# Optimization experiments

Hardware: AMD Instinct MI355X
Metric: run time of the kernel (lower is better)

## Reference

```python
import jax, jax.numpy as jnp
import numpy as np

EPS_NORM = 1e-12  # torch F.normalize eps


def _resize_bilinear_ac(x, H, W):
    # Bilinear resize with align_corners=True on NCHW tensor x.
    h, w = x.shape[-2], x.shape[-1]
    ys = jnp.linspace(0.0, h - 1.0, H)
    xs = jnp.linspace(0.0, w - 1.0, W)
    y0 = jnp.floor(ys).astype(jnp.int32); y1 = jnp.minimum(y0 + 1, h - 1)
    x0 = jnp.floor(xs).astype(jnp.int32); x1 = jnp.minimum(x0 + 1, w - 1)
    wy = (ys - y0).astype(x.dtype)[None, None, :, None]
    wx = (xs - x0).astype(x.dtype)
    rows = x[:, :, y0, :] * (1 - wy) + x[:, :, y1, :] * wy  # (B,C,H,w)
    return rows[:, :, :, x0] * (1 - wx) + rows[:, :, :, x1] * wx  # (B,C,H,W)


def _icc(p, b):
    # p: (b, 19, hw) row-stochastic over hw.
    # M[i, j] = KLDiv(input=p_i, target=p_j, batchmean) = (1/b) * sum p_j*(log p_j - p_i)
    # NOTE: original code passes probabilities (not log-probs) as KLDiv input; kept faithful.
    E = jnp.sum(p * jnp.log(p), axis=(0, 2))            # (19,) sum_b,k p log p
    G = jnp.einsum('bik,bjk->ij', p, p)                  # (19,19) sum_b,k p_i p_j
    M = (E[None, :] - G) / b
    sym = jnp.triu(M) + jnp.triu(M, 1).T                 # loop writes value for i<=j to both [i,j],[j,i]
    nrm = jnp.maximum(jnp.linalg.norm(sym, axis=1, keepdims=True), EPS_NORM)
    return sym / nrm                                     # F.normalize(dim=1)


def reference(s_out, t_out, t_logit, s_logit, conv_w, conv_b):
    T = 1.0  # temperature
    # --- pi_loss ---
    B, C, H, W = t_out.shape
    s1 = _resize_bilinear_ac(s_out, H, W)
    s1 = jnp.einsum('bchw,oc->bohw', s1, conv_w[:, :, 0, 0]) + conv_b[None, :, None, None]
    log_ps = jax.nn.log_softmax(s1 / T, axis=1)
    pt = jax.nn.softmax(t_out / T, axis=1)
    # torch KLDivLoss() default reduction='mean' (mean over ALL elements)
    pi_loss = jnp.mean(pt * (jnp.log(pt) - log_ps))
    # --- lo_loss ---
    b, n, h, w = s_logit.shape
    tl = _resize_bilinear_ac(t_logit, h, w)
    s = jax.nn.softmax(s_logit.reshape(b, n, h * w) / T, axis=2)
    t = jax.nn.softmax(tl.reshape(b, n, h * w) / T, axis=2)
    ICCS = _icc(s, b)
    ICCT = _icc(t, b)
    lo_loss = jnp.sum((ICCS - ICCT) ** 2)
    return pi_loss, lo_loss


def setup_inputs() -> dict:
    key = jax.random.key(0)
    k = jax.random.split(key, 6)
    return {
        's_out': jax.random.normal(k[0], (8, 128, 33, 33), jnp.float32),
        't_out': jax.random.normal(k[1], (8, 768, 65, 65), jnp.float32),
        't_logit': jax.random.normal(k[2], (8, 19, 65, 65), jnp.float32),
        's_logit': jax.random.normal(k[3], (8, 19, 129, 129), jnp.float32),
        'conv_w': jax.random.normal(k[4], (768, 128, 1, 1), jnp.float32) * 0.05,
        'conv_b': jax.random.normal(k[5], (768,), jnp.float32) * 0.05,
    }
```

## Files before the change

### kernel.cpp

```cpp
#include <hip/hip_runtime.h>
#include <math.h>

#define WS_E0   0
#define WS_E1   19
#define WS_G0   64
#define WS_G1   448
#define WS_Z    1152
#define WS_WBF  2048
#define WS_PART 51200

typedef __bf16 bf16x8 __attribute__((ext_vector_type(8)));
typedef float  f32x4  __attribute__((ext_vector_type(4)));
typedef const __attribute__((address_space(1))) unsigned int guint;
typedef       __attribute__((address_space(3))) unsigned int luint;

__global__ void k_init(const float* __restrict__ conv_w, float* __restrict__ ws,
                       float* __restrict__ out) {
    const int bx = blockIdx.x, tid = threadIdx.x;
    if (bx < 96) {
        __bf16* Wb = (__bf16*)(ws + WS_WBF);
        #pragma unroll
        for (int j = 0; j < 4; j++) {
            int idx = bx * 1024 + j * 256 + tid;
            Wb[idx] = (__bf16)conv_w[idx];
        }
    } else {
        for (int k = tid; k < 2048; k += 256) ws[k] = 0.f;
        if (tid < 2) out[tid] = 0.f;
    }
}

__device__ __forceinline__ float t_resized(const float* __restrict__ Trow, int k) {
    int y = k / 129, x = k - y * 129;
    int y0 = y >> 1, x0 = x >> 1;
    int y1 = y0 + (y & 1), x1 = x0 + (x & 1);
    float fy = 0.5f * (float)(y & 1), fx = 0.5f * (float)(x & 1);
    float v00 = Trow[y0 * 65 + x0], v01 = Trow[y0 * 65 + x1];
    float v10 = Trow[y1 * 65 + x0], v11 = Trow[y1 * 65 + x1];
    float r0 = v00 + fx * (v01 - v00);
    float r1 = v10 + fx * (v11 - v10);
    return r0 + fy * (r1 - r0);
}

__launch_bounds__(256, 2)
__global__ void k_main(const float* __restrict__ s_out, const float* __restrict__ t_out,
                       const float* __restrict__ conv_w, const float* __restrict__ bias,
                       const float* __restrict__ s_logit, const float* __restrict__ t_logit,
                       float* __restrict__ ws, float* __restrict__ out) {
    __shared__ __align__(16) char lds[67584];
    const int tid = threadIdx.x;
    const int bx  = blockIdx.x;

    if (bx >= 304 && bx < 1360) {
        const int idx     = bx - 304;
        const int quarter = idx & 3;
        const int bs      = idx >> 2;
        const int b       = bs / 33;
        const int strip   = bs - b * 33;
        const int px0     = strip * 128;

        __bf16* xs = (__bf16*)lds;

        {
            const float* Sb = s_out + b * 128 * 1089;
            #pragma unroll
            for (int ii = 0; ii < 64; ii++) {
                int id2 = tid + ii * 256;
                int c = id2 >> 7, px = id2 & 127;
                int hw = px0 + px;
                int h = hw / 65, w = hw - h * 65;
                int y0 = h >> 1, x0 = w >> 1;
                int y1 = y0 + (h & 1), x1 = x0 + (w & 1);
                float wy = 0.5f * (float)(h & 1), wx = 0.5f * (float)(w & 1);
                const float* Sc = Sb + c * 1089;
                float v00 = Sc[y0 * 33 + x0], v01 = Sc[y0 * 33 + x1];
                float v10 = Sc[y1 * 33 + x0], v11 = Sc[y1 * 33 + x1];
                float r0 = v00 + wx * (v01 - v00);
                float r1 = v10 + wx * (v11 - v10);
                xs[px * 136 + c] = (__bf16)(r0 + wy * (r1 - r0));
            }
        }
        __syncthreads();

        const int l = tid & 63, g = tid >> 6, q = l >> 4, n = l & 15;

        bf16x8 bfrag[8][4];
        #pragma unroll
        for (int pt = 0; pt < 8; pt++)
            #pragma unroll
            for (int kf = 0; kf < 4; kf++)
                bfrag[pt][kf] = *(const bf16x8*)&xs[(pt * 16 + n) * 136 + kf * 32 + q * 8];
        __syncthreads();

        const __bf16* Wbf = (const __bf16*)(ws + WS_WBF);
        const int og = quarter * 192 + g * 16;

        const float* gbl = t_out + ((size_t)(b * 768 + og)) * 4225 + px0 + l;
        char* lbw = lds + g * 8448;
        auto issue_t = [&](int cc, int sel) {
            const float* gb = gbl + (size_t)cc * 64 * 4225;
            char* lb = lbw + sel * 33792;
            #pragma unroll
            for (int r = 0; r < 16; r++) {
                __builtin_amdgcn_global_load_lds((guint*)(gb + (size_t)r * 4225),
                                                 (luint*)(lb + r * 528), 4, 0, 0);
                __builtin_amdgcn_global_load_lds((guint*)(gb + (size_t)r * 4225 + 64),
                                                 (luint*)(lb + r * 528 + 256), 4, 0, 0);
            }
        };
        auto load_a = [&](int cc, bf16x8* afr, f32x4& bqv) {
            const __bf16* Wr = Wbf + (size_t)(og + cc * 64 + n) * 128 + q * 8;
            #pragma unroll
            for (int kf = 0; kf < 4; kf++) afr[kf] = *(const bf16x8*)(Wr + kf * 32);
            bqv = *(const f32x4*)&bias[og + cc * 64 + q * 4];
        };

        bf16x8 afr[2][4];
        f32x4  bq[2];
        load_a(0, afr[0], bq[0]);
        issue_t(0, 0);

        float Zt[8], St[8], Dd[8], Zs[8];
        #pragma unroll
        for (int pt = 0; pt < 8; pt++) { Zt[pt] = 0.f; St[pt] = 0.f; Dd[pt] = 0.f; Zs[pt] = 0.f; }

        for (int c = 0; c < 3; c++) {
            const int cur = c & 1;
            asm volatile("s_waitcnt vmcnt(0)" ::: "memory");
            if (c < 2) { load_a(c + 1, afr[1 - cur], bq[1 - cur]); issue_t(c + 1, 1 - cur); }

            const float* tw = (const float*)(lbw + cur * 33792);
            #pragma unroll
            for (int pt = 0; pt < 8; pt++) {
                f32x4 a0 = {0.f, 0.f, 0.f, 0.f};
                #pragma unroll
                for (int kf = 0; kf < 4; kf++)
                    a0 = __builtin_amdgcn_mfma_f32_16x16x32_bf16(afr[cur][kf], bfrag[pt][kf], a0, 0, 0, 0);
                #pragma unroll
                for (int r = 0; r < 4; r++) {
                    float tv  = tw[(q * 4 + r) * 132 + pt * 16 + n];
                    float s1v = a0[r] + bq[cur][r];
                    float e   = __expf(tv);
                    Zt[pt] += e;
                    St[pt]  = fmaf(e, tv,  St[pt]);
                    Dd[pt]  = fmaf(e, s1v, Dd[pt]);
                    Zs[pt] += __expf(s1v);
                }
            }
        }

        __syncthreads();
        float* scr = (float*)lds;
        {
            int p = g * 4 + q;
            #pragma unroll
            for (int pt = 0; pt < 8; pt++) {
                f32x4 v = {Zt[pt], St[pt], Dd[pt], Zs[pt]};
                *(f32x4*)&scr[(pt * 16 + n) * 68 + p * 4] = v;
            }
        }
        __syncthreads();
        if (tid < 128) {
            float Z = 0.f, S = 0.f, D = 0.f, Z2 = 0.f;
            #pragma unroll
            for (int p = 0; p < 16; p++) {
                f32x4 v = *(const f32x4*)&scr[tid * 68 + p * 4];
                Z += v[0]; S += v[1]; D += v[2]; Z2 += v[3];
            }
            f32x4 o4 = {Z, S, D, Z2};
            *(f32x4*)&ws[WS_PART + (((size_t)quarter * 8 + b) * 4224 + px0 + tid) * 4] = o4;
        }
    } else if (bx < 304) {
        float* red = (float*)lds;
        int row  = bx;
        int side = (row >= 152) ? 1 : 0;
        int r    = side ? row - 152 : row;
        const float* src = side ? (t_logit + r * 4225) : (s_logit + r * 16641);

        float z = 0.f, s = 0.f;
        for (int k = tid; k < 16641; k += 256) {
            float v = side ? t_resized(src, k) : src[k];
            float e = __expf(v);
            z += e;
            s = fmaf(e, v, s);
        }
        for (int off = 32; off > 0; off >>= 1) { z += __shfl_down(z, off); s += __shfl_down(s, off); }
        if ((tid & 63) == 0) { red[tid >> 6] = z; red[4 + (tid >> 6)] = s; }
        __syncthreads();
        if (tid == 0) {
            float Z = red[0] + red[1] + red[2] + red[3];
            float S = red[4] + red[5] + red[6] + red[7];
            ws[WS_Z + row] = Z;
            atomicAdd(&ws[(side ? WS_E1 : WS_E0) + (r % 19)], S / Z - logf(Z));
        }
    } else {
        float* xc  = (float*)lds;
        float* red = (float*)lds + 128;
        const int b = bx - 1360;
        if (tid < 128) xc[tid] = s_out[((size_t)b * 128 + tid) * 1089 + 1088];
        __syncthreads();
        float z = 0.f, s = 0.f, d = 0.f, z2 = 0.f;
        #pragma unroll
        for (int rep = 0; rep < 3; rep++) {
            int o = tid + rep * 256;
            const float* Wr = conv_w + (size_t)o * 128;
            float s1 = bias[o];
            for (int cc = 0; cc < 128; cc++) s1 = fmaf(Wr[cc], xc[cc], s1);
            float tv = t_out[((size_t)(b * 768 + o)) * 4225 + 4224];
            float e  = __expf(tv);
            z += e; s = fmaf(e, tv, s); d = fmaf(e, s1, d); z2 += __expf(s1);
        }
        for (int off = 32; off > 0; off >>= 1) {
            z += __shfl_down(z, off); s += __shfl_down(s, off);
            d += __shfl_down(d, off); z2 += __shfl_down(z2, off);
        }
        if ((tid & 63) == 0) {
            int wv = tid >> 6;
            red[wv] = z; red[4 + wv] = s; red[8 + wv] = d; red[12 + wv] = z2;
        }
        __syncthreads();
        if (tid == 0) {
            float Z = red[0] + red[1] + red[2] + red[3];
            float S = red[4] + red[5] + red[6] + red[7];
            float D = red[8] + red[9] + red[10] + red[11];
            float Z2 = red[12] + red[13] + red[14] + red[15];
            float contrib = (S - D) / Z - logf(Z) + logf(Z2);
            atomicAdd(out, contrib * (1.0f / 25958400.0f));
        }
    }
}

#define KT 512
#define KP 516
__global__ void k_mid(const float* __restrict__ s_logit, const float* __restrict__ t_logit,
                      float* __restrict__ ws, float* __restrict__ out) {
    __shared__ __align__(16) char lds[39296];
    const int tid = threadIdx.x;
    const int bx  = blockIdx.x;

    if (bx < 528) {
        float* pbuf  = (float*)lds;
        float* rowiz = (float*)(lds + 39216);
        int side = (bx >= 264) ? 1 : 0;
        int rm   = side ? bx - 264 : bx;
        int b = rm / 33, kt = rm - b * 33;
        int k0 = kt * KT;

        if (tid < 19) rowiz[tid] = 1.0f / ws[WS_Z + side * 152 + b * 19 + tid];
        __syncthreads();

        for (int i = 0; i < 19; i++) {
            const float* src = side ? (t_logit + (b * 19 + i) * 4225) : (s_logit + (b * 19 + i) * 16641);
            float iz = rowiz[i];
            for (int kl = tid; kl < KT; kl += 256) {
                int k = k0 + kl;
                float p = 0.f;
                if (k < 16641) {
                    float v = side ? t_resized(src, k) : src[k];
                    p = __expf(v) * iz;
                }
                pbuf[i * KP + kl] = p;
            }
        }
        __syncthreads();

        if (tid < 190) {
            int t = tid, i = 0;
            while (t >= 19 - i) { t -= 19 - i; i++; }
            int j = i + t;
            const float* pi_ = &pbuf[i * KP];
            const float* pj_ = &pbuf[j * KP];
            float g = 0.f;
            #pragma unroll 4
            for (int kl = 0; kl < KT; kl += 4) {
                float4 a = *(const float4*)&pi_[kl];
                float4 c = *(const float4*)&pj_[kl];
                g = fmaf(a.x, c.x, g); g = fmaf(a.y, c.y, g);
                g = fmaf(a.z, c.z, g); g = fmaf(a.w, c.w, g);
            }
            atomicAdd(&ws[(side ? WS_G1 : WS_G0) + i * 19 + j], g);
        }
    } else {
        float* red = (float*)lds;
        int gp = (bx - 528) * 256 + tid;
        int b  = gp / 4224;
        int tp = gp - b * 4224;
        float Z = 0.f, S = 0.f, D = 0.f, Z2 = 0.f;
        #pragma unroll
        for (int qq = 0; qq < 4; qq++) {
            f32x4 v = *(const f32x4*)&ws[WS_PART + (((size_t)qq * 8 + b) * 4224 + tp) * 4];
            Z += v[0]; S += v[1]; D += v[2]; Z2 += v[3];
        }
        float contrib = (S - D) / Z - logf(Z) + logf(Z2);
        for (int off = 32; off > 0; off >>= 1) contrib += __shfl_down(contrib, off);
        if ((tid & 63) == 0) red[tid >> 6] = contrib;
        __syncthreads();
        if (tid == 0)
            atomicAdd(out, (red[0] + red[1] + red[2] + red[3]) * (1.0f / 25958400.0f));
    }
}

__global__ void k_final(const float* __restrict__ ws, float* __restrict__ out) {
    __shared__ float Ms[361], Mt[361], ns[19], nt[19];
    __shared__ float red[8];
    int tid = threadIdx.x;
    if (tid < 361) {
        int i = tid / 19, j = tid - i * 19;
        int lo = min(i, j), hi = max(i, j);
        Ms[tid] = (ws[WS_E0 + hi] - ws[WS_G0 + lo * 19 + hi]) * 0.125f;
        Mt[tid] = (ws[WS_E1 + hi] - ws[WS_G1 + lo * 19 + hi]) * 0.125f;
    }
    __syncthreads();
    if (tid < 19) {
        float as = 0.f, at = 0.f;
        for (int j = 0; j < 19; j++) {
            as = fmaf(Ms[tid * 19 + j], Ms[tid * 19 + j], as);
            at = fmaf(Mt[tid * 19 + j], Mt[tid * 19 + j], at);
        }
        ns[tid] = fmaxf(sqrtf(as), 1e-12f);
        nt[tid] = fmaxf(sqrtf(at), 1e-12f);
    }
    __syncthreads();
    float d = 0.f;
    if (tid < 361) {
        int i = tid / 19;
        float v = Ms[tid] / ns[i] - Mt[tid] / nt[i];
        d = v * v;
    }
    for (int off = 32; off > 0; off >>= 1) d += __shfl_down(d, off);
    if ((tid & 63) == 0) red[tid >> 6] = d;
    __syncthreads();
    if (tid == 0) out[1] = red[0] + red[1] + red[2] + red[3] + red[4] + red[5];
}

extern "C" void kernel_launch(void* const* d_in, const int* in_sizes, int n_in,
                              void* d_out, int out_size, void* d_ws, size_t ws_size,
                              hipStream_t stream) {
    const float* s_out   = (const float*)d_in[0];
    const float* t_out   = (const float*)d_in[1];
    const float* t_logit = (const float*)d_in[2];
    const float* s_logit = (const float*)d_in[3];
    const float* conv_w  = (const float*)d_in[4];
    const float* conv_b  = (const float*)d_in[5];
    float* out = (float*)d_out;
    float* ws  = (float*)d_ws;

    k_init<<<dim3(97), dim3(256), 0, stream>>>(conv_w, ws, out);
    k_main<<<dim3(1368), dim3(256), 0, stream>>>(s_out, t_out, conv_w, conv_b,
                                                 s_logit, t_logit, ws, out);
    k_mid<<<dim3(660), dim3(256), 0, stream>>>(s_logit, t_logit, ws, out);
    k_final<<<dim3(1), dim3(384), 0, stream>>>(ws, out);
}
```

Measured before the change: 277.0 us.

## Halve pixel strips, use 16-byte LDS-direct loads, raise occupancy to three blocks

Shrinks each main-block pixel strip from 128 to 64 pixels, doubling the block count and cutting LDS and register use so three blocks fit per CU. The t_out tile loads switch from 4-byte global_load_lds ops to 16-byte ones with a swizzled column layout, and all three weight chunks are preloaded up front. A partial vmcnt wait lets the next chunk's loads overlap compute. The intent is better latency hiding and fewer load instructions, at the cost of more blocks that each redo the per-strip resize of s_out.

```diff
diff --git a/kernel.cpp b/kernel.cpp
--- a/kernel.cpp
+++ b/kernel.cpp
@@ -42,31 +42,31 @@
     return r0 + fy * (r1 - r0);
 }
 
-__launch_bounds__(256, 2)
+__launch_bounds__(256, 3)
 __global__ void k_main(const float* __restrict__ s_out, const float* __restrict__ t_out,
                        const float* __restrict__ conv_w, const float* __restrict__ bias,
                        const float* __restrict__ s_logit, const float* __restrict__ t_logit,
                        float* __restrict__ ws, float* __restrict__ out) {
-    __shared__ __align__(16) char lds[67584];
+    __shared__ __align__(16) char lds[50176];
     const int tid = threadIdx.x;
     const int bx  = blockIdx.x;
 
-    if (bx >= 304 && bx < 1360) {
+    if (bx >= 304 && bx < 2416) {
         const int idx     = bx - 304;
         const int quarter = idx & 3;
         const int bs      = idx >> 2;
-        const int b       = bs / 33;
-        const int strip   = bs - b * 33;
-        const int px0     = strip * 128;
+        const int b       = bs / 66;
+        const int strip   = bs - b * 66;
+        const int px0     = strip * 64;
 
         __bf16* xs = (__bf16*)lds;
 
         {
             const float* Sb = s_out + b * 128 * 1089;
             #pragma unroll
-            for (int ii = 0; ii < 64; ii++) {
+            for (int ii = 0; ii < 32; ii++) {
                 int id2 = tid + ii * 256;
-                int c = id2 >> 7, px = id2 & 127;
+                int c = id2 >> 6, px = id2 & 63;
                 int hw = px0 + px;
                 int h = hw / 65, w = hw - h * 65;
                 int y0 = h >> 1, x0 = w >> 1;
@@ -83,63 +83,73 @@
         __syncthreads();
 
         const int l = tid & 63, g = tid >> 6, q = l >> 4, n = l & 15;
-
-        bf16x8 bfrag[8][4];
-        #pragma unroll
-        for (int pt = 0; pt < 8; pt++)
+        const int m = n;
+
+        bf16x8 bfrag[4][4];
+        #pragma unroll
+        for (int pt = 0; pt < 4; pt++)
             #pragma unroll
             for (int kf = 0; kf < 4; kf++)
                 bfrag[pt][kf] = *(const bf16x8*)&xs[(pt * 16 + n) * 136 + kf * 32 + q * 8];
-        __syncthreads();
 
         const __bf16* Wbf = (const __bf16*)(ws + WS_WBF);
         const int og = quarter * 192 + g * 16;
-
-        const float* gbl = t_out + ((size_t)(b * 768 + og)) * 4225 + px0 + l;
-        char* lbw = lds + g * 8448;
+        bf16x8 afr[3][4];
+        f32x4  bq[3];
+        #pragma unroll
+        for (int c = 0; c < 3; c++) {
+            const __bf16* Wr = Wbf + (size_t)(og + c * 64 + n) * 128 + q * 8;
+            #pragma unroll
+            for (int kf = 0; kf < 4; kf++) afr[c][kf] = *(const bf16x8*)(Wr + kf * 32);
+            bq[c] = *(const f32x4*)&bias[og + c * 64 + q * 4];
+        }
+
+        const float* base_t = t_out + (size_t)(b * 768 + og) * 4225;
+        int off[4];
+        #pragma unroll
+        for (int j = 0; j < 4; j++) {
+            int col = ((m * 4) + j * 16) & 63;
+            off[j] = (j * 4 + q) * 4225 + px0 + col;
+        }
+        int colr[4];
+        #pragma unroll
+        for (int pt = 0; pt < 4; pt++)
+            colr[pt] = (((pt * 16 + (n & 12) - q * 16) & 63)) + (n & 3);
+
+        char* lbw = lds + 17408 + g * 4096;
         auto issue_t = [&](int cc, int sel) {
-            const float* gb = gbl + (size_t)cc * 64 * 4225;
-            char* lb = lbw + sel * 33792;
-            #pragma unroll
-            for (int r = 0; r < 16; r++) {
-                __builtin_amdgcn_global_load_lds((guint*)(gb + (size_t)r * 4225),
-                                                 (luint*)(lb + r * 528), 4, 0, 0);
-                __builtin_amdgcn_global_load_lds((guint*)(gb + (size_t)r * 4225 + 64),
-                                                 (luint*)(lb + r * 528 + 256), 4, 0, 0);
-            }
+            char* lb = lbw + sel * 16384;
+            #pragma unroll
+            for (int j = 0; j < 4; j++)
+                __builtin_amdgcn_global_load_lds((guint*)(base_t + off[j] + cc * 270400),
+                                                 (luint*)(lb + j * 1024), 16, 0, 0);
         };
-        auto load_a = [&](int cc, bf16x8* afr, f32x4& bqv) {
-            const __bf16* Wr = Wbf + (size_t)(og + cc * 64 + n) * 128 + q * 8;
-            #pragma unroll
-            for (int kf = 0; kf < 4; kf++) afr[kf] = *(const bf16x8*)(Wr + kf * 32);
-            bqv = *(const f32x4*)&bias[og + cc * 64 + q * 4];
-        };
-
-        bf16x8 afr[2][4];
-        f32x4  bq[2];
-        load_a(0, afr[0], bq[0]);
+
+        float Zt[4], St[4], Dd[4], Zs[4];
+        #pragma unroll
+        for (int pt = 0; pt < 4; pt++) { Zt[pt] = 0.f; St[pt] = 0.f; Dd[pt] = 0.f; Zs[pt] = 0.f; }
+
         issue_t(0, 0);
-
-        float Zt[8], St[8], Dd[8], Zs[8];
-        #pragma unroll
-        for (int pt = 0; pt < 8; pt++) { Zt[pt] = 0.f; St[pt] = 0.f; Dd[pt] = 0.f; Zs[pt] = 0.f; }
-
+        #pragma unroll
         for (int c = 0; c < 3; c++) {
             const int cur = c & 1;
-            asm volatile("s_waitcnt vmcnt(0)" ::: "memory");
-            if (c < 2) { load_a(c + 1, afr[1 - cur], bq[1 - cur]); issue_t(c + 1, 1 - cur); }
-
-            const float* tw = (const float*)(lbw + cur * 33792);
-            #pragma unroll
-            for (int pt = 0; pt < 8; pt++) {
+            if (c < 2) {
+                issue_t(c + 1, 1 - cur);
+                asm volatile("s_waitcnt vmcnt(4)" ::: "memory");
+            } else {
+                asm volatile("s_waitcnt vmcnt(0)" ::: "memory");
+            }
+            const float* tw = (const float*)(lbw + cur * 16384);
+            #pragma unroll
+            for (int pt = 0; pt < 4; pt++) {
                 f32x4 a0 = {0.f, 0.f, 0.f, 0.f};
                 #pragma unroll
                 for (int kf = 0; kf < 4; kf++)
-                    a0 = __builtin_amdgcn_mfma_f32_16x16x32_bf16(afr[cur][kf], bfrag[pt][kf], a0, 0, 0, 0);
+                    a0 = __builtin_amdgcn_mfma_f32_16x16x32_bf16(afr[c][kf], bfrag[pt][kf], a0, 0, 0, 0);
                 #pragma unroll
                 for (int r = 0; r < 4; r++) {
-                    float tv  = tw[(q * 4 + r) * 132 + pt * 16 + n];
-                    float s1v = a0[r] + bq[cur][r];
+                    float tv  = tw[(q * 4 + r) * 64 + colr[pt]];
+                    float s1v = a0[r] + bq[c][r];
                     float e   = __expf(tv);
                     Zt[pt] += e;
                     St[pt]  = fmaf(e, tv,  St[pt]);
@@ -154,13 +164,13 @@
         {
             int p = g * 4 + q;
             #pragma unroll
-            for (int pt = 0; pt < 8; pt++) {
+            for (int pt = 0; pt < 4; pt++) {
                 f32x4 v = {Zt[pt], St[pt], Dd[pt], Zs[pt]};
                 *(f32x4*)&scr[(pt * 16 + n) * 68 + p * 4] = v;
             }
         }
         __syncthreads();
-        if (tid < 128) {
+        if (tid < 64) {
             float Z = 0.f, S = 0.f, D = 0.f, Z2 = 0.f;
             #pragma unroll
             for (int p = 0; p < 16; p++) {
@@ -196,7 +206,7 @@
     } else {
         float* xc  = (float*)lds;
         float* red = (float*)lds + 128;
-        const int b = bx - 1360;
+        const int b = bx - 2416;
         if (tid < 128) xc[tid] = s_out[((size_t)b * 128 + tid) * 1089 + 1088];
         __syncthreads();
         float z = 0.f, s = 0.f, d = 0.f, z2 = 0.f;
@@ -346,7 +356,7 @@
     float* ws  = (float*)d_ws;
 
     k_init<<<dim3(97), dim3(256), 0, stream>>>(conv_w, ws, out);
-    k_main<<<dim3(1368), dim3(256), 0, stream>>>(s_out, t_out, conv_w, conv_b,
+    k_main<<<dim3(2424), dim3(256), 0, stream>>>(s_out, t_out, conv_w, conv_b,
                                                  s_logit, t_logit, ws, out);
     k_mid<<<dim3(660), dim3(256), 0, stream>>>(s_logit, t_logit, ws, out);
     k_final<<<dim3(1), dim3(384), 0, stream>>>(ws, out);
```

Result: faster. 245.8 us (-11.3%).
